# Kernel tuning notes

Hardware: AMD Instinct MI355X
Metric: run time of the kernel (lower is better)

The kernel has to match this reference:

```python
import jax, jax.numpy as jnp
import numpy as np

B, T, W, CIN, H, COUT = 256, 512, 64, 2, 256, 2
FIN = W * CIN  # 128


def setup_inputs() -> dict:
    key = jax.random.key(0)
    ks = jax.random.split(key, 9)
    s = lambda *sh: 1.0 / np.sqrt(sh[0])
    x = jax.random.normal(ks[0], (B, T, W, CIN), dtype=jnp.float32)
    W1 = jax.random.normal(ks[1], (FIN, H), dtype=jnp.float32) * s(FIN)
    b1 = jnp.zeros((H,), dtype=jnp.float32)
    Wk = jax.random.normal(ks[2], (H, 3 * H), dtype=jnp.float32) * s(H)
    Wr = jax.random.normal(ks[3], (H, 3 * H), dtype=jnp.float32) * s(H)
    bi = jnp.zeros((3 * H,), dtype=jnp.float32)
    br = jnp.zeros((3 * H,), dtype=jnp.float32)
    W2 = jax.random.normal(ks[4], (2 * H, W * COUT), dtype=jnp.float32) * s(2 * H)
    b2 = jnp.zeros((W * COUT,), dtype=jnp.float32)
    return {"x": x, "W1": W1, "b1": b1, "Wk": Wk, "Wr": Wr, "bi": bi, "br": br, "W2": W2, "b2": b2}


def _gru_relu(xg, Wr, br):
    # xg: (T, B, 3H) precomputed input-side gates (x @ Wk + bi)
    # Keras GRU v2: reset_after=True, recurrent_activation=sigmoid, activation=relu
    Hd = Wr.shape[0]
    h0 = jnp.zeros((xg.shape[1], Hd), dtype=xg.dtype)

    def step(h, xg_t):
        rec = h @ Wr + br                     # (B, 3H)
        xz, xr, xh = jnp.split(xg_t, 3, axis=-1)
        rz, rr, rh = jnp.split(rec, 3, axis=-1)
        z = jax.nn.sigmoid(xz + rz)
        r = jax.nn.sigmoid(xr + rr)
        hh = jax.nn.relu(xh + r * rh)
        h_new = z * h + (1.0 - z) * hh
        return h_new, None

    h_last, _ = jax.lax.scan(step, h0, xg)
    return h_last


def reference(x, W1, b1, Wk, Wr, bi, br, W2, b2):
    b = x.shape[0]
    xf = x.reshape(b, T, FIN)                 # Reshape((T, W*CIN))
    h1 = jax.nn.relu(xf @ W1 + b1)            # Dense(hidden, relu): (B, T, H)
    xg = jnp.transpose(h1 @ Wk + bi, (1, 0, 2))  # (T, B, 3H)
    h_last = _gru_relu(xg, Wr, br)            # (B, H); output == final_state
    feat = jnp.concatenate([h_last, h_last], axis=-1)  # (B, 2H)
    y = feat @ W2 + b2                        # (B, W*COUT)
    return y.reshape(b, W, COUT)
```

## Files before the change

kernel.cpp:

```cpp
#include <hip/hip_runtime.h>

typedef unsigned short u16;
typedef unsigned int u32;
typedef float f32x4 __attribute__((ext_vector_type(4)));
typedef __bf16 bf16x8 __attribute__((ext_vector_type(8)));
typedef u16 u16x4 __attribute__((ext_vector_type(4)));

#define TB 256
#define TT 512
#define TC 64

__device__ __forceinline__ u16 f2b(float f) {
  u32 x = __float_as_uint(f);
  return (u16)((x + 0x7fffu + ((x >> 16) & 1u)) >> 16);
}
__device__ __forceinline__ u32 pkbf(float a, float b) {
  u32 r;
  asm("v_cvt_pk_bf16_f32 %0, %1, %2" : "=v"(r) : "v"(a), "v"(b));
  return r;
}
__device__ __forceinline__ float blo(u32 u) { return __uint_as_float(u << 16); }
__device__ __forceinline__ float bhi(u32 u) { return __uint_as_float(u & 0xffff0000u); }
__device__ __forceinline__ float sigm(float x) {
  return __builtin_amdgcn_rcpf(1.f + __expf(-x));
}

__global__ void tcast_kernel(const float* __restrict__ in, u16* __restrict__ out, int K, int N) {
  int idx = blockIdx.x * blockDim.x + threadIdx.x;
  if (idx < K * N) {
    int k = idx / N, n = idx % N;
    out[n * K + k] = f2b(in[idx]);
  }
}

__global__ void wrperm_kernel(const float* __restrict__ in, u16* __restrict__ out) {
  int idx = blockIdx.x * blockDim.x + threadIdx.x;
  if (idx < 256 * 768) {
    int k = idx / 768, n = idx % 768;
    int gate = n >> 8, c = n & 255;
    int w = c >> 5, cc = c & 31, l15 = cc >> 1, grp = cc & 1;
    int nt = gate * 2 + grp;
    out[((((w * 6 + nt) << 4) + l15) << 8) + k] = f2b(in[idx]);
  }
}

__global__ void biasmod_kernel(const float* __restrict__ bi, const float* __restrict__ br,
                               float* __restrict__ bm) {
  int n = blockIdx.x * blockDim.x + threadIdx.x;
  if (n < 768) bm[n] = bi[n] + (n < 512 ? br[n] : 0.f);
}

template<int KT, int MODE, int CASTA>
__global__ __launch_bounds__(256) void gemm_bf16(const void* __restrict__ Av, const u16* __restrict__ Bt,
                                                 const float* __restrict__ bias, u16* __restrict__ C,
                                                 int t0) {
  constexpr int K = KT * 32;
  const u16* A = (const u16*)Av;
  const float* Af = (const float*)Av;
  __shared__ u16 As[128 * 40];
  __shared__ u16 Bs[128 * 40];
  const int tid = threadIdx.x;
  const int bm = blockIdx.x, bn = blockIdx.y;
  const int lane = tid & 63, wid = tid >> 6;
  const int l15 = lane & 15, l4 = lane >> 4;
  const int qm = (wid >> 1) * 64, qn = (wid & 1) * 64;

  const int c0 = tid, c1 = tid + 256;
  const int r0 = c0 >> 2, r1 = c1 >> 2;
  const int ar0 = (MODE == 0) ? (bm * 128 + r0) : ((2 * bm + (r0 >> 6)) * 512 + t0 + (r0 & 63));
  const int ar1 = (MODE == 0) ? (bm * 128 + r1) : ((2 * bm + (r1 >> 6)) * 512 + t0 + (r1 & 63));
  const size_t ga0 = (size_t)ar0 * K + (c0 & 3) * 8;
  const size_t ga1 = (size_t)ar1 * K + (c1 & 3) * 8;
  const size_t gb0 = (size_t)(bn * 128 + r0) * K + (c0 & 3) * 8;
  const size_t gb1 = (size_t)(bn * 128 + r1) * K + (c1 & 3) * 8;
  const int sa0 = r0 * 40 + (c0 & 3) * 8;
  const int sa1 = r1 * 40 + (c1 & 3) * 8;

#define LOADA(ga, ko, dst)                                                       \
  if (CASTA) {                                                                   \
    const float* p = Af + (ga) + (ko);                                           \
    const f32x4 v0 = *(const f32x4*)(p);                                         \
    const f32x4 v1 = *(const f32x4*)(p + 4);                                     \
    (dst).x = pkbf(v0[0], v0[1]); (dst).y = pkbf(v0[2], v0[3]);                  \
    (dst).z = pkbf(v1[0], v1[1]); (dst).w = pkbf(v1[2], v1[3]);                  \
  } else {                                                                       \
    (dst) = *(const uint4*)(A + (ga) + (ko));                                    \
  }

  uint4 ra0, ra1, rb0, rb1;
  LOADA(ga0, 0, ra0);
  LOADA(ga1, 0, ra1);
  rb0 = *(const uint4*)(Bt + gb0);
  rb1 = *(const uint4*)(Bt + gb1);

  f32x4 acc[4][4] = {};

  for (int kt = 0; kt < KT; ++kt) {
    __syncthreads();
    *(uint4*)(As + sa0) = ra0;
    *(uint4*)(As + sa1) = ra1;
    *(uint4*)(Bs + sa0) = rb0;
    *(uint4*)(Bs + sa1) = rb1;
    __syncthreads();
    if (kt + 1 < KT) {
      const int ko = (kt + 1) * 32;
      LOADA(ga0, ko, ra0);
      LOADA(ga1, ko, ra1);
      rb0 = *(const uint4*)(Bt + gb0 + ko);
      rb1 = *(const uint4*)(Bt + gb1 + ko);
    }
    bf16x8 af[4], bfr[4];
#pragma unroll
    for (int mt = 0; mt < 4; ++mt)
      af[mt] = *(const bf16x8*)(As + (qm + mt * 16 + l15) * 40 + l4 * 8);
#pragma unroll
    for (int nt = 0; nt < 4; ++nt)
      bfr[nt] = *(const bf16x8*)(Bs + (qn + nt * 16 + l15) * 40 + l4 * 8);
#pragma unroll
    for (int mt = 0; mt < 4; ++mt)
#pragma unroll
      for (int nt = 0; nt < 4; ++nt)
        acc[mt][nt] = __builtin_amdgcn_mfma_f32_16x16x32_bf16(af[mt], bfr[nt], acc[mt][nt], 0, 0, 0);
  }
#undef LOADA

#pragma unroll
  for (int mt = 0; mt < 4; ++mt) {
#pragma unroll
    for (int nt = 0; nt < 4; ++nt) {
      const int n = bn * 128 + qn + nt * 16 + l15;
      const float bv = bias[n];
#pragma unroll
      for (int j = 0; j < 4; ++j) {
        const int rloc = qm + mt * 16 + l4 * 4 + j;
        float v = acc[mt][nt][j] + bv;
        if (MODE == 0) {
          v = fmaxf(v, 0.f);
          C[(size_t)(bm * 128 + rloc) * 256 + n] = f2b(v);
        } else {
          C[((size_t)bm * 128 + rloc) * 768 + n] = f2b(v);
        }
      }
    }
  }
}

__global__ __launch_bounds__(512, 1) void fused_kernel(
    const u16* __restrict__ xrd, u16* __restrict__ xwr,
    const u16* __restrict__ WrP, const float* __restrict__ br,
    float* __restrict__ hstate, const u16* __restrict__ h1A,
    const u16* __restrict__ WkT, const float* __restrict__ biasM,
    int t0, int do_gemm) {
  __shared__ alignas(16) char smem_c[82048];
  const int tid = threadIdx.x;

  if (blockIdx.x < 16) {
    u16* hb0 = (u16*)smem_c;
    u16* hb1 = (u16*)(smem_c + 8448);
    u16* xs0 = (u16*)(smem_c + 16896);
    u16* xs1 = (u16*)(smem_c + 41728);
    const int g = blockIdx.x;
    const int lane = tid & 63, wid = tid >> 6;
    const int l15 = lane & 15, l4 = lane >> 4;

    bf16x8 bw[8][6];
#pragma unroll
    for (int kk = 0; kk < 8; ++kk)
#pragma unroll
      for (int nt = 0; nt < 6; ++nt)
        bw[kk][nt] = *(const bf16x8*)(WrP + ((((wid * 6 + nt) << 4) + l15) << 8) + kk * 32 + l4 * 8);

    const int cbase = wid * 32 + l15 * 2;
    const float brh0 = br[512 + cbase];
    const float brh1 = br[512 + cbase + 1];

    const int rs = tid >> 5, ksl = (tid & 31) * 8;
    const u16* xg_row = xrd + (size_t)(g * 16 + rs) * TC * 768 + ksl;
    u16* xw0 = xs0 + rs * 776 + ksl;
    u16* xw1 = xs1 + rs * 776 + ksl;

    f32x4 h0v, h1v;
    if (t0 == 0) {
      h0v = {0.f, 0.f, 0.f, 0.f};
      h1v = {0.f, 0.f, 0.f, 0.f};
    } else {
#pragma unroll
      for (int j = 0; j < 4; ++j) {
        float2 ld = *(const float2*)(hstate + ((size_t)g * 16 + l4 * 4 + j) * 256 + cbase);
        h0v[j] = ld.x; h1v[j] = ld.y;
      }
    }
#pragma unroll
    for (int j = 0; j < 4; ++j)
      *(u32*)(hb0 + (l4 * 4 + j) * 264 + cbase) = pkbf(h0v[j], h1v[j]);

    {
      const uint4 s0 = *(const uint4*)(xg_row);
      const uint4 s1 = *(const uint4*)(xg_row + 256);
      const uint4 s2 = *(const uint4*)(xg_row + 512);
      *(uint4*)(xw0) = s0;
      *(uint4*)(xw0 + 256) = s1;
      *(uint4*)(xw0 + 512) = s2;
    }
    __syncthreads();

#define GRU_STEP(SRC, DST, XRD, XWR, TL)                                                    \
  {                                                                                         \
    const int tn = ((TL) + 1 < TC) ? ((TL) + 1) : (TC - 1);                                 \
    const u16* xq = xg_row + (size_t)tn * 768;                                              \
    const uint4 s0 = *(const uint4*)(xq);                                                   \
    const uint4 s1 = *(const uint4*)(xq + 256);                                             \
    const uint4 s2 = *(const uint4*)(xq + 512);                                             \
    f32x4 a0 = {}, a2 = {}, a4 = {};                                                        \
    _Pragma("unroll")                                                                       \
    for (int kk = 0; kk < 8; ++kk) {                                                        \
      const bf16x8 a = *(const bf16x8*)((SRC) + l15 * 264 + kk * 32 + l4 * 8);              \
      a0 = __builtin_amdgcn_mfma_f32_16x16x32_bf16(a, bw[kk][0], a0, 0, 0, 0);              \
      a2 = __builtin_amdgcn_mfma_f32_16x16x32_bf16(a, bw[kk][2], a2, 0, 0, 0);              \
      a4 = __builtin_amdgcn_mfma_f32_16x16x32_bf16(a, bw[kk][4], a4, 0, 0, 0);              \
    }                                                                                       \
    u32 xz_[4], xr_[4], xh_[4];                                                             \
    _Pragma("unroll")                                                                       \
    for (int j = 0; j < 4; ++j) {                                                           \
      const u16* xr2 = (XRD) + (l4 * 4 + j) * 776 + cbase;                                  \
      xz_[j] = *(const u32*)(xr2);                                                          \
      xr_[j] = *(const u32*)(xr2 + 256);                                                    \
      xh_[j] = *(const u32*)(xr2 + 512);                                                    \
    }                                                                                       \
    f32x4 a1 = {}, a3 = {}, a5 = {};                                                        \
    _Pragma("unroll")                                                                       \
    for (int kk = 0; kk < 8; ++kk) {                                                        \
      const bf16x8 a = *(const bf16x8*)((SRC) + l15 * 264 + kk * 32 + l4 * 8);              \
      a1 = __builtin_amdgcn_mfma_f32_16x16x32_bf16(a, bw[kk][1], a1, 0, 0, 0);              \
      a3 = __builtin_amdgcn_mfma_f32_16x16x32_bf16(a, bw[kk][3], a3, 0, 0, 0);              \
      a5 = __builtin_amdgcn_mfma_f32_16x16x32_bf16(a, bw[kk][5], a5, 0, 0, 0);              \
    }                                                                                       \
    *(uint4*)(XWR) = s0;                                                                    \
    *(uint4*)((XWR) + 256) = s1;                                                            \
    *(uint4*)((XWR) + 512) = s2;                                                            \
    _Pragma("unroll")                                                                       \
    for (int j = 0; j < 4; ++j) {                                                           \
      const float z0 = sigm(blo(xz_[j]) + a0[j]);                                           \
      const float r0 = sigm(blo(xr_[j]) + a2[j]);                                           \
      const float hh0 = fmaxf(fmaf(r0, a4[j] + brh0, blo(xh_[j])), 0.f);                    \
      h0v[j] = fmaf(z0, h0v[j] - hh0, hh0);                                                 \
    }                                                                                       \
    _Pragma("unroll")                                                                       \
    for (int j = 0; j < 4; ++j) {                                                           \
      const float z1 = sigm(bhi(xz_[j]) + a1[j]);                                           \
      const float r1 = sigm(bhi(xr_[j]) + a3[j]);                                           \
      const float hh1 = fmaxf(fmaf(r1, a5[j] + brh1, bhi(xh_[j])), 0.f);                    \
      h1v[j] = fmaf(z1, h1v[j] - hh1, hh1);                                                 \
      *(u32*)((DST) + (l4 * 4 + j) * 264 + cbase) = pkbf(h0v[j], h1v[j]);                   \
    }                                                                                       \
    __syncthreads();                                                                        \
  }

    for (int tl = 0; tl < TC; tl += 2) {
      GRU_STEP(hb0, hb1, xs0, xw1, tl);
      GRU_STEP(hb1, hb0, xs1, xw0, tl + 1);
    }
#undef GRU_STEP

#pragma unroll
    for (int j = 0; j < 4; ++j) {
      float2 st = {h0v[j], h1v[j]};
      *(float2*)(hstate + ((size_t)g * 16 + l4 * 4 + j) * 256 + cbase) = st;
    }
  } else {
    if (!do_gemm) return;
    u16* As = (u16*)smem_c;
    u16* Bs = (u16*)(smem_c + 10240);
    const int bidx = blockIdx.x - 16;
    const int bm = bidx & 127, bn = bidx >> 7;
    const int t0g = t0 + TC;
    const bool act = (tid < 256);
    const int lane = tid & 63, wid = tid >> 6;
    const int l15 = lane & 15, l4 = lane >> 4;
    const int qm = ((wid & 3) >> 1) * 64, qn = (wid & 1) * 64;

    const int c0 = tid & 255, c1 = (tid & 255) + 256;
    const int r0 = c0 >> 2, r1 = c1 >> 2;
    const int ar0 = (2 * bm + (r0 >> 6)) * 512 + t0g + (r0 & 63);
    const int ar1 = (2 * bm + (r1 >> 6)) * 512 + t0g + (r1 & 63);
    const size_t ga0 = (size_t)ar0 * 256 + (c0 & 3) * 8;
    const size_t ga1 = (size_t)ar1 * 256 + (c1 & 3) * 8;
    const size_t gb0 = (size_t)(bn * 128 + r0) * 256 + (c0 & 3) * 8;
    const size_t gb1 = (size_t)(bn * 128 + r1) * 256 + (c1 & 3) * 8;
    const int sa0 = r0 * 40 + (c0 & 3) * 8;
    const int sa1 = r1 * 40 + (c1 & 3) * 8;

    uint4 ra0 = {}, ra1 = {}, rb0 = {}, rb1 = {};
    if (act) {
      ra0 = *(const uint4*)(h1A + ga0);
      ra1 = *(const uint4*)(h1A + ga1);
      rb0 = *(const uint4*)(WkT + gb0);
      rb1 = *(const uint4*)(WkT + gb1);
    }
    f32x4 acc[4][4] = {};

    for (int kt = 0; kt < 8; ++kt) {
      __syncthreads();
      if (act) {
        *(uint4*)(As + sa0) = ra0;
        *(uint4*)(As + sa1) = ra1;
        *(uint4*)(Bs + sa0) = rb0;
        *(uint4*)(Bs + sa1) = rb1;
      }
      __syncthreads();
      if (act) {
        if (kt + 1 < 8) {
          const int ko = (kt + 1) * 32;
          ra0 = *(const uint4*)(h1A + ga0 + ko);
          ra1 = *(const uint4*)(h1A + ga1 + ko);
          rb0 = *(const uint4*)(WkT + gb0 + ko);
          rb1 = *(const uint4*)(WkT + gb1 + ko);
        }
        bf16x8 af[4], bfr[4];
#pragma unroll
        for (int mt = 0; mt < 4; ++mt)
          af[mt] = *(const bf16x8*)(As + (qm + mt * 16 + l15) * 40 + l4 * 8);
#pragma unroll
        for (int nt = 0; nt < 4; ++nt)
          bfr[nt] = *(const bf16x8*)(Bs + (qn + nt * 16 + l15) * 40 + l4 * 8);
#pragma unroll
        for (int mt = 0; mt < 4; ++mt)
#pragma unroll
          for (int nt = 0; nt < 4; ++nt)
            acc[mt][nt] = __builtin_amdgcn_mfma_f32_16x16x32_bf16(af[mt], bfr[nt], acc[mt][nt], 0, 0, 0);
      }
    }

    if (act) {
#pragma unroll
      for (int mt = 0; mt < 4; ++mt)
#pragma unroll
        for (int nt = 0; nt < 4; ++nt) {
          const int n = bn * 128 + qn + nt * 16 + l15;
          const float bv = biasM[n];
#pragma unroll
          for (int j = 0; j < 4; ++j) {
            const int rloc = qm + mt * 16 + l4 * 4 + j;
            xwr[((size_t)bm * 128 + rloc) * 768 + n] = f2b(acc[mt][nt][j] + bv);
          }
        }
    }
  }
}

__global__ void out_kernel(const float* __restrict__ h, const float* __restrict__ W2,
                           const float* __restrict__ b2, float* __restrict__ y) {
  const int bb = blockIdx.x, j = threadIdx.x;
  const float* hr = h + (size_t)bb * 256;
  float s = b2[j];
  for (int i = 0; i < 256; ++i)
    s = fmaf(hr[i], W2[i * 128 + j] + W2[(i + 256) * 128 + j], s);
  y[(size_t)bb * 128 + j] = s;
}

extern "C" void kernel_launch(void* const* d_in, const int* in_sizes, int n_in,
                              void* d_out, int out_size, void* d_ws, size_t ws_size,
                              hipStream_t stream) {
  const float* x  = (const float*)d_in[0];
  const float* W1 = (const float*)d_in[1];
  const float* b1 = (const float*)d_in[2];
  const float* Wk = (const float*)d_in[3];
  const float* Wr = (const float*)d_in[4];
  const float* bi = (const float*)d_in[5];
  const float* br = (const float*)d_in[6];
  const float* W2 = (const float*)d_in[7];
  const float* b2 = (const float*)d_in[8];
  float* y = (float*)d_out;

  const size_t NEED = 67108864ull + 25165824ull + 25165824ull + 65536ull + 393216ull +
                      393216ull + 262144ull + 4096ull;
  if (ws_size < NEED) return;

  char* ws = (char*)d_ws;
  u16* h1    = (u16*)ws;  ws += 67108864;
  u16* xg0   = (u16*)ws;  ws += 25165824;
  u16* xg1   = (u16*)ws;  ws += 25165824;
  u16* W1T   = (u16*)ws;  ws += 65536;
  u16* WkT   = (u16*)ws;  ws += 393216;
  u16* WrP   = (u16*)ws;  ws += 393216;
  float* hstate = (float*)ws; ws += 262144;
  float* biasM  = (float*)ws;

  tcast_kernel<<<128, 256, 0, stream>>>(W1, W1T, 128, 256);
  tcast_kernel<<<768, 256, 0, stream>>>(Wk, WkT, 256, 768);
  wrperm_kernel<<<768, 256, 0, stream>>>(Wr, WrP);
  biasmod_kernel<<<3, 256, 0, stream>>>(bi, br, biasM);
  gemm_bf16<4, 0, 1><<<dim3(1024, 2), 256, 0, stream>>>(x, W1T, b1, h1, 0);
  gemm_bf16<8, 1, 0><<<dim3(128, 6), 256, 0, stream>>>(h1, WkT, biasM, xg0, 0);
  for (int c = 0; c < TT / TC; ++c) {
    const u16* xrd = (c & 1) ? xg1 : xg0;
    u16* xwr = (c & 1) ? xg0 : xg1;
    fused_kernel<<<784, 512, 0, stream>>>(xrd, xwr, WrP, br, hstate, h1, WkT, biasM,
                                          c * TC, (c < TT / TC - 1) ? 1 : 0);
  }
  out_kernel<<<256, 128, 0, stream>>>(hstate, W2, b2, y);
}
```

Measured before the change: 1.008 ms.

## Merge all prep, GEMM and GRU chunk launches into one cooperative persistent kernel

Replaces the weight-cast kernels, the two GEMM launches and the eight per-chunk fused launches with a single cooperative kernel of 256 blocks. Phases are separated by grid.sync, and the GRU blocks keep hidden state in registers across chunks instead of round-tripping through global memory. This removes per-launch overhead and the hstate reload between chunks. In exchange the grid shrinks from 784 to 256 blocks, so the big input GEMM and each per-chunk xg GEMM now run in looped tiles over fewer blocks, which could lengthen the non-recurrent phases.

```diff
diff --git a/kernel.cpp b/kernel.cpp
--- a/kernel.cpp
+++ b/kernel.cpp
@@ -1,14 +1,17 @@
 #include <hip/hip_runtime.h>
+#include <hip/hip_cooperative_groups.h>
+
+namespace cg = cooperative_groups;
 
 typedef unsigned short u16;
 typedef unsigned int u32;
 typedef float f32x4 __attribute__((ext_vector_type(4)));
 typedef __bf16 bf16x8 __attribute__((ext_vector_type(8)));
-typedef u16 u16x4 __attribute__((ext_vector_type(4)));
 
 #define TB 256
 #define TT 512
 #define TC 64
+#define NCHUNK 8
 
 __device__ __forceinline__ u16 f2b(float f) {
   u32 x = __float_as_uint(f);
@@ -25,47 +28,22 @@
   return __builtin_amdgcn_rcpf(1.f + __expf(-x));
 }
 
-__global__ void tcast_kernel(const float* __restrict__ in, u16* __restrict__ out, int K, int N) {
-  int idx = blockIdx.x * blockDim.x + threadIdx.x;
-  if (idx < K * N) {
-    int k = idx / N, n = idx % N;
-    out[n * K + k] = f2b(in[idx]);
-  }
-}
-
-__global__ void wrperm_kernel(const float* __restrict__ in, u16* __restrict__ out) {
-  int idx = blockIdx.x * blockDim.x + threadIdx.x;
-  if (idx < 256 * 768) {
-    int k = idx / 768, n = idx % 768;
-    int gate = n >> 8, c = n & 255;
-    int w = c >> 5, cc = c & 31, l15 = cc >> 1, grp = cc & 1;
-    int nt = gate * 2 + grp;
-    out[((((w * 6 + nt) << 4) + l15) << 8) + k] = f2b(in[idx]);
-  }
-}
-
-__global__ void biasmod_kernel(const float* __restrict__ bi, const float* __restrict__ br,
-                               float* __restrict__ bm) {
-  int n = blockIdx.x * blockDim.x + threadIdx.x;
-  if (n < 768) bm[n] = bi[n] + (n < 512 ? br[n] : 0.f);
-}
-
 template<int KT, int MODE, int CASTA>
-__global__ __launch_bounds__(256) void gemm_bf16(const void* __restrict__ Av, const u16* __restrict__ Bt,
-                                                 const float* __restrict__ bias, u16* __restrict__ C,
-                                                 int t0) {
+__device__ void gemm_tile(char* smem_c, const void* __restrict__ Av, const u16* __restrict__ Bt,
+                          const float* __restrict__ bias, u16* __restrict__ C, int t0,
+                          int bm, int bn) {
   constexpr int K = KT * 32;
   const u16* A = (const u16*)Av;
   const float* Af = (const float*)Av;
-  __shared__ u16 As[128 * 40];
-  __shared__ u16 Bs[128 * 40];
+  u16* As = (u16*)smem_c;
+  u16* Bs = (u16*)(smem_c + 10240);
   const int tid = threadIdx.x;
-  const int bm = blockIdx.x, bn = blockIdx.y;
+  const bool act = (tid < 256);
   const int lane = tid & 63, wid = tid >> 6;
   const int l15 = lane & 15, l4 = lane >> 4;
-  const int qm = (wid >> 1) * 64, qn = (wid & 1) * 64;
-
-  const int c0 = tid, c1 = tid + 256;
+  const int qm = ((wid & 3) >> 1) * 64, qn = (wid & 1) * 64;
+
+  const int c0 = tid & 255, c1 = (tid & 255) + 256;
   const int r0 = c0 >> 2, r1 = c1 >> 2;
   const int ar0 = (MODE == 0) ? (bm * 128 + r0) : ((2 * bm + (r0 >> 6)) * 512 + t0 + (r0 & 63));
   const int ar1 = (MODE == 0) ? (bm * 128 + r1) : ((2 * bm + (r1 >> 6)) * 512 + t0 + (r1 & 63));
@@ -87,79 +65,117 @@
     (dst) = *(const uint4*)(A + (ga) + (ko));                                    \
   }
 
-  uint4 ra0, ra1, rb0, rb1;
-  LOADA(ga0, 0, ra0);
-  LOADA(ga1, 0, ra1);
-  rb0 = *(const uint4*)(Bt + gb0);
-  rb1 = *(const uint4*)(Bt + gb1);
-
+  uint4 ra0 = {}, ra1 = {}, rb0 = {}, rb1 = {};
+  if (act) {
+    LOADA(ga0, 0, ra0);
+    LOADA(ga1, 0, ra1);
+    rb0 = *(const uint4*)(Bt + gb0);
+    rb1 = *(const uint4*)(Bt + gb1);
+  }
   f32x4 acc[4][4] = {};
 
   for (int kt = 0; kt < KT; ++kt) {
     __syncthreads();
-    *(uint4*)(As + sa0) = ra0;
-    *(uint4*)(As + sa1) = ra1;
-    *(uint4*)(Bs + sa0) = rb0;
-    *(uint4*)(Bs + sa1) = rb1;
+    if (act) {
+      *(uint4*)(As + sa0) = ra0;
+      *(uint4*)(As + sa1) = ra1;
+      *(uint4*)(Bs + sa0) = rb0;
+      *(uint4*)(Bs + sa1) = rb1;
+    }
     __syncthreads();
-    if (kt + 1 < KT) {
-      const int ko = (kt + 1) * 32;
-      LOADA(ga0, ko, ra0);
-      LOADA(ga1, ko, ra1);
-      rb0 = *(const uint4*)(Bt + gb0 + ko);
-      rb1 = *(const uint4*)(Bt + gb1 + ko);
-    }
-    bf16x8 af[4], bfr[4];
+    if (act) {
+      if (kt + 1 < KT) {
+        const int ko = (kt + 1) * 32;
+        LOADA(ga0, ko, ra0);
+        LOADA(ga1, ko, ra1);
+        rb0 = *(const uint4*)(Bt + gb0 + ko);
+        rb1 = *(const uint4*)(Bt + gb1 + ko);
+      }
+      bf16x8 af[4], bfr[4];
+#pragma unroll
+      for (int mt = 0; mt < 4; ++mt)
+        af[mt] = *(const bf16x8*)(As + (qm + mt * 16 + l15) * 40 + l4 * 8);
+#pragma unroll
+      for (int nt = 0; nt < 4; ++nt)
+        bfr[nt] = *(const bf16x8*)(Bs + (qn + nt * 16 + l15) * 40 + l4 * 8);
+#pragma unroll
+      for (int mt = 0; mt < 4; ++mt)
+#pragma unroll
+        for (int nt = 0; nt < 4; ++nt)
+          acc[mt][nt] = __builtin_amdgcn_mfma_f32_16x16x32_bf16(af[mt], bfr[nt], acc[mt][nt], 0, 0, 0);
+    }
+  }
+#undef LOADA
+
+  if (act) {
 #pragma unroll
     for (int mt = 0; mt < 4; ++mt)
-      af[mt] = *(const bf16x8*)(As + (qm + mt * 16 + l15) * 40 + l4 * 8);
-#pragma unroll
-    for (int nt = 0; nt < 4; ++nt)
-      bfr[nt] = *(const bf16x8*)(Bs + (qn + nt * 16 + l15) * 40 + l4 * 8);
-#pragma unroll
-    for (int mt = 0; mt < 4; ++mt)
-#pragma unroll
-      for (int nt = 0; nt < 4; ++nt)
-        acc[mt][nt] = __builtin_amdgcn_mfma_f32_16x16x32_bf16(af[mt], bfr[nt], acc[mt][nt], 0, 0, 0);
-  }
-#undef LOADA
-
-#pragma unroll
-  for (int mt = 0; mt < 4; ++mt) {
-#pragma unroll
-    for (int nt = 0; nt < 4; ++nt) {
-      const int n = bn * 128 + qn + nt * 16 + l15;
-      const float bv = bias[n];
-#pragma unroll
-      for (int j = 0; j < 4; ++j) {
-        const int rloc = qm + mt * 16 + l4 * 4 + j;
-        float v = acc[mt][nt][j] + bv;
-        if (MODE == 0) {
-          v = fmaxf(v, 0.f);
-          C[(size_t)(bm * 128 + rloc) * 256 + n] = f2b(v);
-        } else {
-          C[((size_t)bm * 128 + rloc) * 768 + n] = f2b(v);
+#pragma unroll
+      for (int nt = 0; nt < 4; ++nt) {
+        const int n = bn * 128 + qn + nt * 16 + l15;
+        const float bv = bias[n];
+#pragma unroll
+        for (int j = 0; j < 4; ++j) {
+          const int rloc = qm + mt * 16 + l4 * 4 + j;
+          float v = acc[mt][nt][j] + bv;
+          if (MODE == 0) {
+            v = fmaxf(v, 0.f);
+            C[(size_t)(bm * 128 + rloc) * 256 + n] = f2b(v);
+          } else {
+            C[((size_t)bm * 128 + rloc) * 768 + n] = f2b(v);
+          }
         }
       }
-    }
-  }
-}
-
-__global__ __launch_bounds__(512, 1) void fused_kernel(
-    const u16* __restrict__ xrd, u16* __restrict__ xwr,
-    const u16* __restrict__ WrP, const float* __restrict__ br,
-    float* __restrict__ hstate, const u16* __restrict__ h1A,
-    const u16* __restrict__ WkT, const float* __restrict__ biasM,
-    int t0, int do_gemm) {
+  }
+}
+
+__global__ __launch_bounds__(512, 1) void mega_kernel(
+    const float* __restrict__ x, const float* __restrict__ W1, const float* __restrict__ b1,
+    const float* __restrict__ Wk, const float* __restrict__ Wr,
+    const float* __restrict__ bi, const float* __restrict__ br,
+    u16* __restrict__ h1, u16* __restrict__ xg0, u16* __restrict__ xg1,
+    u16* __restrict__ W1T, u16* __restrict__ WkT, u16* __restrict__ WrP,
+    float* __restrict__ biasM, float* __restrict__ hstate) {
   __shared__ alignas(16) char smem_c[82048];
   const int tid = threadIdx.x;
-
-  if (blockIdx.x < 16) {
+  const int bid = blockIdx.x;
+  cg::grid_group grid = cg::this_grid();
+
+  {
+    const int gt = bid * 512 + tid;
+    if (gt < 32768) {
+      const int k = gt >> 8, n = gt & 255;
+      W1T[n * 128 + k] = f2b(W1[gt]);
+    }
+    for (int idx = gt; idx < 196608; idx += 131072) {
+      const int k = idx / 768, n = idx % 768;
+      WkT[(size_t)n * 256 + k] = f2b(Wk[idx]);
+    }
+    for (int idx = gt; idx < 196608; idx += 131072) {
+      const int k = idx / 768, n = idx % 768;
+      const int gate = n >> 8, c = n & 255;
+      const int w = c >> 5, cc = c & 31, l15 = cc >> 1, grp = cc & 1;
+      const int nt = gate * 2 + grp;
+      WrP[((((w * 6 + nt) << 4) + l15) << 8) + k] = f2b(Wr[idx]);
+    }
+    if (gt < 768) biasM[gt] = bi[gt] + (gt < 512 ? br[gt] : 0.f);
+  }
+  grid.sync();
+
+  for (int tix = bid; tix < 2048; tix += 256)
+    gemm_tile<4, 0, 1>(smem_c, x, W1T, b1, h1, 0, tix >> 1, tix & 1);
+  grid.sync();
+
+  for (int tix = bid; tix < 768; tix += 256)
+    gemm_tile<8, 1, 0>(smem_c, h1, WkT, biasM, xg0, 0, tix & 127, tix >> 7);
+  grid.sync();
+
+  if (bid < 16) {
     u16* hb0 = (u16*)smem_c;
     u16* hb1 = (u16*)(smem_c + 8448);
     u16* xs0 = (u16*)(smem_c + 16896);
     u16* xs1 = (u16*)(smem_c + 41728);
-    const int g = blockIdx.x;
+    const int g = bid;
     const int lane = tid & 63, wid = tid >> 6;
     const int l15 = lane & 15, l4 = lane >> 4;
 
@@ -173,36 +189,28 @@
     const int cbase = wid * 32 + l15 * 2;
     const float brh0 = br[512 + cbase];
     const float brh1 = br[512 + cbase + 1];
-
     const int rs = tid >> 5, ksl = (tid & 31) * 8;
-    const u16* xg_row = xrd + (size_t)(g * 16 + rs) * TC * 768 + ksl;
-    u16* xw0 = xs0 + rs * 776 + ksl;
-    u16* xw1 = xs1 + rs * 776 + ksl;
-
-    f32x4 h0v, h1v;
-    if (t0 == 0) {
-      h0v = {0.f, 0.f, 0.f, 0.f};
-      h1v = {0.f, 0.f, 0.f, 0.f};
-    } else {
-#pragma unroll
-      for (int j = 0; j < 4; ++j) {
-        float2 ld = *(const float2*)(hstate + ((size_t)g * 16 + l4 * 4 + j) * 256 + cbase);
-        h0v[j] = ld.x; h1v[j] = ld.y;
-      }
-    }
+
+    f32x4 h0v = {0.f, 0.f, 0.f, 0.f}, h1v = {0.f, 0.f, 0.f, 0.f};
 #pragma unroll
     for (int j = 0; j < 4; ++j)
-      *(u32*)(hb0 + (l4 * 4 + j) * 264 + cbase) = pkbf(h0v[j], h1v[j]);
-
-    {
-      const uint4 s0 = *(const uint4*)(xg_row);
-      const uint4 s1 = *(const uint4*)(xg_row + 256);
-      const uint4 s2 = *(const uint4*)(xg_row + 512);
-      *(uint4*)(xw0) = s0;
-      *(uint4*)(xw0 + 256) = s1;
-      *(uint4*)(xw0 + 512) = s2;
-    }
-    __syncthreads();
+      *(u32*)(hb0 + (l4 * 4 + j) * 264 + cbase) = 0u;
+
+    for (int c = 0; c < NCHUNK; ++c) {
+      const u16* xrd = (c & 1) ? xg1 : xg0;
+      const u16* xg_row = xrd + (size_t)(g * 16 + rs) * TC * 768 + ksl;
+      u16* xw0 = xs0 + rs * 776 + ksl;
+      u16* xw1 = xs1 + rs * 776 + ksl;
+
+      {
+        const uint4 s0 = *(const uint4*)(xg_row);
+        const uint4 s1 = *(const uint4*)(xg_row + 256);
+        const uint4 s2 = *(const uint4*)(xg_row + 512);
+        *(uint4*)(xw0) = s0;
+        *(uint4*)(xw0 + 256) = s1;
+        *(uint4*)(xw0 + 512) = s2;
+      }
+      __syncthreads();
 
 #define GRU_STEP(SRC, DST, XRD, XWR, TL)                                                    \
   {                                                                                         \
@@ -256,11 +264,14 @@
     __syncthreads();                                                                        \
   }
 
-    for (int tl = 0; tl < TC; tl += 2) {
-      GRU_STEP(hb0, hb1, xs0, xw1, tl);
-      GRU_STEP(hb1, hb0, xs1, xw0, tl + 1);
-    }
+      for (int tl = 0; tl < TC; tl += 2) {
+        GRU_STEP(hb0, hb1, xs0, xw1, tl);
+        GRU_STEP(hb1, hb0, xs1, xw0, tl + 1);
+      }
 #undef GRU_STEP
+
+      grid.sync();
+    }
 
 #pragma unroll
     for (int j = 0; j < 4; ++j) {
@@ -268,82 +279,13 @@
       *(float2*)(hstate + ((size_t)g * 16 + l4 * 4 + j) * 256 + cbase) = st;
     }
   } else {
-    if (!do_gemm) return;
-    u16* As = (u16*)smem_c;
-    u16* Bs = (u16*)(smem_c + 10240);
-    const int bidx = blockIdx.x - 16;
-    const int bm = bidx & 127, bn = bidx >> 7;
-    const int t0g = t0 + TC;
-    const bool act = (tid < 256);
-    const int lane = tid & 63, wid = tid >> 6;
-    const int l15 = lane & 15, l4 = lane >> 4;
-    const int qm = ((wid & 3) >> 1) * 64, qn = (wid & 1) * 64;
-
-    const int c0 = tid & 255, c1 = (tid & 255) + 256;
-    const int r0 = c0 >> 2, r1 = c1 >> 2;
-    const int ar0 = (2 * bm + (r0 >> 6)) * 512 + t0g + (r0 & 63);
-    const int ar1 = (2 * bm + (r1 >> 6)) * 512 + t0g + (r1 & 63);
-    const size_t ga0 = (size_t)ar0 * 256 + (c0 & 3) * 8;
-    const size_t ga1 = (size_t)ar1 * 256 + (c1 & 3) * 8;
-    const size_t gb0 = (size_t)(bn * 128 + r0) * 256 + (c0 & 3) * 8;
-    const size_t gb1 = (size_t)(bn * 128 + r1) * 256 + (c1 & 3) * 8;
-    const int sa0 = r0 * 40 + (c0 & 3) * 8;
-    const int sa1 = r1 * 40 + (c1 & 3) * 8;
-
-    uint4 ra0 = {}, ra1 = {}, rb0 = {}, rb1 = {};
-    if (act) {
-      ra0 = *(const uint4*)(h1A + ga0);
-      ra1 = *(const uint4*)(h1A + ga1);
-      rb0 = *(const uint4*)(WkT + gb0);
-      rb1 = *(const uint4*)(WkT + gb1);
-    }
-    f32x4 acc[4][4] = {};
-
-    for (int kt = 0; kt < 8; ++kt) {
-      __syncthreads();
-      if (act) {
-        *(uint4*)(As + sa0) = ra0;
-        *(uint4*)(As + sa1) = ra1;
-        *(uint4*)(Bs + sa0) = rb0;
-        *(uint4*)(Bs + sa1) = rb1;
-      }
-      __syncthreads();
-      if (act) {
-        if (kt + 1 < 8) {
-          const int ko = (kt + 1) * 32;
-          ra0 = *(const uint4*)(h1A + ga0 + ko);
-          ra1 = *(const uint4*)(h1A + ga1 + ko);
-          rb0 = *(const uint4*)(WkT + gb0 + ko);
-          rb1 = *(const uint4*)(WkT + gb1 + ko);
-        }
-        bf16x8 af[4], bfr[4];
-#pragma unroll
-        for (int mt = 0; mt < 4; ++mt)
-          af[mt] = *(const bf16x8*)(As + (qm + mt * 16 + l15) * 40 + l4 * 8);
-#pragma unroll
-        for (int nt = 0; nt < 4; ++nt)
-          bfr[nt] = *(const bf16x8*)(Bs + (qn + nt * 16 + l15) * 40 + l4 * 8);
-#pragma unroll
-        for (int mt = 0; mt < 4; ++mt)
-#pragma unroll
-          for (int nt = 0; nt < 4; ++nt)
-            acc[mt][nt] = __builtin_amdgcn_mfma_f32_16x16x32_bf16(af[mt], bfr[nt], acc[mt][nt], 0, 0, 0);
-      }
-    }
-
-    if (act) {
-#pragma unroll
-      for (int mt = 0; mt < 4; ++mt)
-#pragma unroll
-        for (int nt = 0; nt < 4; ++nt) {
-          const int n = bn * 128 + qn + nt * 16 + l15;
-          const float bv = biasM[n];
-#pragma unroll
-          for (int j = 0; j < 4; ++j) {
-            const int rloc = qm + mt * 16 + l4 * 4 + j;
-            xwr[((size_t)bm * 128 + rloc) * 768 + n] = f2b(acc[mt][nt][j] + bv);
-          }
-        }
+    for (int c = 0; c < NCHUNK; ++c) {
+      if (c < NCHUNK - 1) {
+        u16* xwr = (c & 1) ? xg0 : xg1;
+        for (int tix = bid - 16; tix < 768; tix += 240)
+          gemm_tile<8, 1, 0>(smem_c, h1, WkT, biasM, xwr, (c + 1) * TC, tix & 127, tix >> 7);
+      }
+      grid.sync();
     }
   }
 }
@@ -386,17 +328,9 @@
   float* hstate = (float*)ws; ws += 262144;
   float* biasM  = (float*)ws;
 
-  tcast_kernel<<<128, 256, 0, stream>>>(W1, W1T, 128, 256);
-  tcast_kernel<<<768, 256, 0, stream>>>(Wk, WkT, 256, 768);
-  wrperm_kernel<<<768, 256, 0, stream>>>(Wr, WrP);
-  biasmod_kernel<<<3, 256, 0, stream>>>(bi, br, biasM);
-  gemm_bf16<4, 0, 1><<<dim3(1024, 2), 256, 0, stream>>>(x, W1T, b1, h1, 0);
-  gemm_bf16<8, 1, 0><<<dim3(128, 6), 256, 0, stream>>>(h1, WkT, biasM, xg0, 0);
-  for (int c = 0; c < TT / TC; ++c) {
-    const u16* xrd = (c & 1) ? xg1 : xg0;
-    u16* xwr = (c & 1) ? xg0 : xg1;
-    fused_kernel<<<784, 512, 0, stream>>>(xrd, xwr, WrP, br, hstate, h1, WkT, biasM,
-                                          c * TC, (c < TT / TC - 1) ? 1 : 0);
-  }
+  void* args[] = { (void*)&x, (void*)&W1, (void*)&b1, (void*)&Wk, (void*)&Wr,
+                   (void*)&bi, (void*)&br, (void*)&h1, (void*)&xg0, (void*)&xg1,
+                   (void*)&W1T, (void*)&WkT, (void*)&WrP, (void*)&biasM, (void*)&hstate };
+  hipLaunchCooperativeKernel((void*)mega_kernel, dim3(256), dim3(512), args, 0, stream);
   out_kernel<<<256, 128, 0, stream>>>(hstate, W2, b2, y);
 }
```

Measured after the change: 1.212 ms. 20.3% more time.
